# Performance work log

Measured on AMD Instinct MI355X. Metric: run time of the kernel, lower is better.

Reference implementation:

```python
import jax, jax.numpy as jnp
import numpy as np

HIDDEN = 1024
HEADS = 16
HEAD_DIM = HIDDEN // HEADS
SCALE = 1.0 / float(np.sqrt(HEAD_DIM))


def setup_inputs() -> dict:
    key = jax.random.key(0)
    k1, k2, k3, k4 = jax.random.split(key, 4)
    B, N, C = 4, 2048, HIDDEN
    x = jax.random.normal(k1, (B, N, C), dtype=jnp.float32)
    # nn.Linear(C, 3C, bias=False): y = x @ W_qkv where W_qkv is [C, 3C]
    w_qkv = jax.random.normal(k2, (C, 3 * C), dtype=jnp.float32) * (1.0 / np.sqrt(C))
    # nn.Linear(C, C) with bias
    w_out = jax.random.normal(k3, (C, C), dtype=jnp.float32) * (1.0 / np.sqrt(C))
    b_out = jax.random.normal(k4, (C,), dtype=jnp.float32) * 0.01
    return {"x": x, "w_qkv": w_qkv, "w_out": w_out, "b_out": b_out}


def reference(x, w_qkv, w_out, b_out):
    B, N, C = x.shape
    H, D = HEADS, HEAD_DIM
    qkv = jnp.einsum("bnc,cf->bnf", x, w_qkv)  # [B, N, 3C]
    qkv = qkv.reshape(B, N, 3, H, D).transpose(2, 0, 3, 1, 4)  # [3, B, H, N, D]
    q, k, v = qkv[0], qkv[1], qkv[2]
    attn = jnp.einsum("bhnd,bhmd->bhnm", q, k) * SCALE  # [B, H, N, N]
    attn = jax.nn.softmax(attn, axis=-1)
    # dropout is identity in eval mode
    out = jnp.einsum("bhnm,bhmd->bhnd", attn, v)  # [B, H, N, D]
    out = out.transpose(0, 2, 1, 3).reshape(B, N, C)
    return jnp.einsum("bnc,co->bno", out, w_out) + b_out
```

## Files before the change

### kernel.cpp

```cpp
#include <hip/hip_runtime.h>
#include <hip/hip_bf16.h>
#include <stdint.h>

#define SEQ   2048
#define NBH   64
#define DH    64
#define CH    1024
#define MTOT  8192
#define QSCALE 0.1803368801111204f

typedef __bf16 bf16_t;
typedef bf16_t bf16x8 __attribute__((ext_vector_type(8)));
typedef float  f32x4  __attribute__((ext_vector_type(4)));
typedef float  f32x16 __attribute__((ext_vector_type(16)));

__device__ __forceinline__ bf16_t to_bf16(float f) {
  uint32_t u = __builtin_bit_cast(uint32_t, f);
  uint16_t r = (uint16_t)((u + 0x7fffu + ((u >> 16) & 1u)) >> 16);
  return __builtin_bit_cast(bf16_t, r);
}

__device__ __forceinline__ void gload_lds16(const void* g, void* l) {
  __builtin_amdgcn_global_load_lds(
      (const __attribute__((address_space(1))) uint32_t*)g,
      (__attribute__((address_space(3))) uint32_t*)l, 16, 0, 0);
}

__device__ __forceinline__ f32x4 mfma_bf16(bf16x8 a, bf16x8 b, f32x4 c) {
  return __builtin_amdgcn_mfma_f32_16x16x32_bf16(a, b, c, 0, 0, 0);
}
__device__ __forceinline__ f32x16 mfma32_bf16(bf16x8 a, bf16x8 b, f32x16 c) {
  return __builtin_amdgcn_mfma_f32_32x32x16_bf16(a, b, c, 0, 0, 0);
}

__device__ __forceinline__ float exp2_fast(float x) {
#if __has_builtin(__builtin_amdgcn_exp2f)
  return __builtin_amdgcn_exp2f(x);
#else
  float r;
  asm("v_exp_f32 %0, %1\ns_nop 0" : "=v"(r) : "v"(x));
  return r;
#endif
}

__device__ __forceinline__ uint32_t cvt_pk_bf16(float lo, float hi) {
  uint32_t r;
  asm("v_cvt_pk_bf16_f32 %0, %1, %2" : "=v"(r) : "v"(lo), "v"(hi));
  return r;
}

__device__ __forceinline__ void permlane32_swap(uint32_t& a, uint32_t& b) {
  asm("s_nop 1\n\tv_permlane32_swap_b32 %0, %1\n\ts_nop 1" : "+v"(a), "+v"(b));
}

__global__ __launch_bounds__(256) void prep(
    const float* __restrict__ x, bf16_t* __restrict__ xb,
    const float* __restrict__ w_qkv, bf16_t* __restrict__ wqkvT,
    const float* __restrict__ w_out, bf16_t* __restrict__ woT) {
  __shared__ float t[64 * 65];
  const int tid = threadIdx.x;
  const int blk = blockIdx.x;
  if (blk < 2048) {
    int i = (blk * 256 + tid) * 8;
    const int stride = 2048 * 256 * 8;
    for (; i < MTOT * CH; i += stride) {
      const float4 f0 = *reinterpret_cast<const float4*>(x + i);
      const float4 f1 = *reinterpret_cast<const float4*>(x + i + 4);
      const uint4 pk = make_uint4(cvt_pk_bf16(f0.x, f0.y), cvt_pk_bf16(f0.z, f0.w),
                                  cvt_pk_bf16(f1.x, f1.y), cvt_pk_bf16(f1.z, f1.w));
      *reinterpret_cast<uint4*>(xb + i) = pk;
    }
    return;
  }
  const float* W; bf16_t* WT; int Nd, nx, bi;
  if (blk < 2048 + 768) { bi = blk - 2048; W = w_qkv; WT = wqkvT; Nd = 3 * CH; nx = 48; }
  else                  { bi = blk - 2816; W = w_out; WT = woT;   Nd = CH;     nx = 16; }
  const int n0 = (bi % nx) * 64, k0 = (bi / nx) * 64;
#pragma unroll
  for (int rr = 0; rr < 16; ++rr) {
    const int idx = rr * 256 + tid;
    const int r = idx >> 6, c = idx & 63;
    t[r * 65 + c] = W[(size_t)(k0 + r) * Nd + n0 + c];
  }
  __syncthreads();
#pragma unroll
  for (int rr = 0; rr < 16; ++rr) {
    const int idx = rr * 256 + tid;
    const int nr = idx >> 6, kc = idx & 63;
    WT[(size_t)(n0 + nr) * CH + k0 + kc] = to_bf16(t[kc * 65 + nr]);
  }
}


template <int EPI>
__global__ __launch_bounds__(256, 3) void gemm_bt(
    const bf16_t* __restrict__ A, const bf16_t* __restrict__ BT, int K, int nx,
    bf16_t* __restrict__ qb, bf16_t* __restrict__ kb, bf16_t* __restrict__ vb,
    const float* __restrict__ bias, float* __restrict__ out) {
  __shared__ __attribute__((aligned(16))) bf16_t lA[128 * 64];
  __shared__ __attribute__((aligned(16))) bf16_t lB[128 * 64];
  const int tid = threadIdx.x;
  const int lane = tid & 63;
  const int wv = tid >> 6;
  const int wm = wv >> 1, wn = wv & 1;

  const int nwg = gridDim.x;
  int bid = blockIdx.x;
  bid = (bid & 7) * (nwg >> 3) + (bid >> 3);
  const int m0 = (bid / nx) * 128, n0 = (bid % nx) * 128;

  const int l15 = lane & 15, l16 = lane >> 4;

  f32x4 acc[4][4] = {};

  const int srow = tid >> 3;
  const int sch = tid & 7;

  for (int kt = 0; kt < K; kt += 64) {
#pragma unroll
    for (int c = 0; c < 4; ++c) {
      const int row = c * 32 + srow;
      const int cs = sch ^ (row & 7);
      gload_lds16(A + (size_t)(m0 + row) * K + kt + cs * 8, &lA[c * 2048 + tid * 8]);
    }
#pragma unroll
    for (int c = 0; c < 4; ++c) {
      const int row = c * 32 + srow;
      const int cs = sch ^ (row & 7);
      gload_lds16(BT + (size_t)(n0 + row) * K + kt + cs * 8, &lB[c * 2048 + tid * 8]);
    }
    __syncthreads();
#pragma unroll
    for (int ks = 0; ks < 2; ++ks) {
      bf16x8 af[4], bfr[4];
#pragma unroll
      for (int i = 0; i < 4; ++i) {
        const int ar = wm * 64 + i * 16 + l15;
        const int cha = (ks * 4 + l16) ^ (ar & 7);
        af[i] = *reinterpret_cast<const bf16x8*>(&lA[ar * 64 + cha * 8]);
        const int br = wn * 64 + i * 16 + l15;
        const int chb = (ks * 4 + l16) ^ (br & 7);
        bfr[i] = *reinterpret_cast<const bf16x8*>(&lB[br * 64 + chb * 8]);
      }
#pragma unroll
      for (int i = 0; i < 4; ++i)
#pragma unroll
        for (int j = 0; j < 4; ++j)
          acc[i][j] = mfma_bf16(af[i], bfr[j], acc[i][j]);
    }
    __syncthreads();
  }

  if (EPI == 0) {
    const int f0 = n0 + wn * 64;
    const int three = f0 >> 10;
    if (three < 2) {
#pragma unroll
      for (int i = 0; i < 4; ++i) {
#pragma unroll
        for (int j = 0; j < 4; ++j) {
#pragma unroll
          for (int r = 0; r < 4; ++r) {
            const int m = m0 + wm * 64 + i * 16 + l16 * 4 + r;
            const int f = f0 + j * 16 + l15;
            const int h = (f >> 6) & 15, d = f & 63;
            const int bh = (m >> 11) * 16 + h;
            const int n = m & 2047;
            const float val = acc[i][j][r];
            if (three == 0)
              qb[((size_t)bh * SEQ + n) * DH + d] = to_bf16(val * QSCALE);
            else
              kb[((size_t)bh * SEQ + n) * DH + d] = to_bf16(val);
          }
        }
      }
    } else {
#pragma unroll
      for (int i = 0; i < 4; ++i) {
#pragma unroll
        for (int j = 0; j < 4; ++j) {
          const int m = m0 + wm * 64 + i * 16 + l16 * 4;
          const int f = f0 + j * 16 + l15;
          const int h = (f >> 6) & 15, d = f & 63;
          const int bh = (m >> 11) * 16 + h;
          const int n = m & 2047;
          const uint2 pk = make_uint2(cvt_pk_bf16(acc[i][j][0], acc[i][j][1]),
                                      cvt_pk_bf16(acc[i][j][2], acc[i][j][3]));
          *reinterpret_cast<uint2*>(&vb[((size_t)bh * DH + d) * SEQ + n]) = pk;
        }
      }
    }
  } else {
#pragma unroll
    for (int j = 0; j < 4; ++j) {
      const int cc = n0 + wn * 64 + j * 16 + l15;
      const float bb = bias[cc];
#pragma unroll
      for (int i = 0; i < 4; ++i) {
#pragma unroll
        for (int r = 0; r < 4; ++r) {
          const int m = m0 + wm * 64 + i * 16 + l16 * 4 + r;
          out[(size_t)m * CH + cc] = acc[i][j][r] + bb;
        }
      }
    }
  }
}

__global__ __launch_bounds__(256, 4) void attn_fwd(
    const bf16_t* __restrict__ Q, const bf16_t* __restrict__ K,
    const bf16_t* __restrict__ V, bf16_t* __restrict__ O) {
  __shared__ __attribute__((aligned(16))) bf16_t lK[2][64 * 64];
  __shared__ __attribute__((aligned(16))) bf16_t lV[2][64 * 64];
  const int tid = threadIdx.x;
  const int lane = tid & 63;
  const int wv = tid >> 6;
  const int l31 = lane & 31, hi = lane >> 5;

  const int lin = blockIdx.x;
  const int bh = (lin & 7) * 8 + ((lin >> 3) & 7);
  const int qb = lin >> 6;
  const int q0w = qb * 128 + wv * 32;

  const bf16_t* Qb = Q + (size_t)bh * SEQ * DH;
  const bf16_t* Kb = K + (size_t)bh * SEQ * DH;
  const bf16_t* Vb = V + (size_t)bh * DH * SEQ;

  bf16x8 qf[4];
#pragma unroll
  for (int ks = 0; ks < 4; ++ks)
    qf[ks] = *reinterpret_cast<const bf16x8*>(
        Qb + (size_t)(q0w + l31) * DH + ks * 16 + hi * 8);

  f32x16 o0 = {}, o1 = {};
  float rs0 = 0.f, rs1 = 0.f, rs2 = 0.f, rs3 = 0.f;

  const int srow = tid >> 3;
  const int sch = tid & 7;

  auto stage = [&](int buf, int kt0) {
#pragma unroll
    for (int c = 0; c < 2; ++c) {
      const int row = c * 32 + srow;
      const int cs = sch ^ (row & 7);
      gload_lds16(Kb + (size_t)(kt0 + row) * DH + cs * 8,
                  reinterpret_cast<char*>(&lK[buf][0]) + c * 4096 + tid * 16);
      gload_lds16(Vb + (size_t)row * SEQ + kt0 + cs * 8,
                  reinterpret_cast<char*>(&lV[buf][0]) + c * 4096 + tid * 16);
    }
  };

  stage(0, 0);
  __syncthreads();
  int cur = 0;

  for (int t = 0; t < SEQ / 64; ++t) {
    if (t + 1 < SEQ / 64) stage(cur ^ 1, (t + 1) * 64);

    f32x16 s0 = {}, s1 = {};
    __builtin_amdgcn_s_setprio(1);
#pragma unroll
    for (int ks = 0; ks < 4; ++ks) {
      {
        const int row = l31;
        const int ch = (ks * 2 + hi) ^ (row & 7);
        const bf16x8 kf = *reinterpret_cast<const bf16x8*>(
            reinterpret_cast<const char*>(&lK[cur][0]) + row * 128 + ch * 16);
        s0 = mfma32_bf16(kf, qf[ks], s0);
      }
      {
        const int row = 32 + l31;
        const int ch = (ks * 2 + hi) ^ (row & 7);
        const bf16x8 kf = *reinterpret_cast<const bf16x8*>(
            reinterpret_cast<const char*>(&lK[cur][0]) + row * 128 + ch * 16);
        s1 = mfma32_bf16(kf, qf[ks], s1);
      }
    }
    __builtin_amdgcn_s_setprio(0);

#pragma unroll
    for (int j = 0; j < 16; j += 4) {
      s0[j]     = exp2_fast(s0[j]);     rs0 += s0[j];
      s0[j + 1] = exp2_fast(s0[j + 1]); rs1 += s0[j + 1];
      s0[j + 2] = exp2_fast(s0[j + 2]); rs2 += s0[j + 2];
      s0[j + 3] = exp2_fast(s0[j + 3]); rs3 += s0[j + 3];
    }
#pragma unroll
    for (int j = 0; j < 16; j += 4) {
      s1[j]     = exp2_fast(s1[j]);     rs0 += s1[j];
      s1[j + 1] = exp2_fast(s1[j + 1]); rs1 += s1[j + 1];
      s1[j + 2] = exp2_fast(s1[j + 2]); rs2 += s1[j + 2];
      s1[j + 3] = exp2_fast(s1[j + 3]); rs3 += s1[j + 3];
    }

    bf16x8 pa[4];
    {
      uint32_t a0 = cvt_pk_bf16(s0[0], s0[1]),   b0 = cvt_pk_bf16(s0[4], s0[5]);
      uint32_t a1 = cvt_pk_bf16(s0[2], s0[3]),   b1 = cvt_pk_bf16(s0[6], s0[7]);
      uint32_t a2 = cvt_pk_bf16(s0[8], s0[9]),   b2 = cvt_pk_bf16(s0[12], s0[13]);
      uint32_t a3 = cvt_pk_bf16(s0[10], s0[11]), b3 = cvt_pk_bf16(s0[14], s0[15]);
      permlane32_swap(a0, b0);
      permlane32_swap(a1, b1);
      permlane32_swap(a2, b2);
      permlane32_swap(a3, b3);
      union { uint32_t u[4]; bf16x8 v; } ua, ub, uc, ud;
      ua.u[0] = a0; ua.u[1] = a1; ua.u[2] = b0; ua.u[3] = b1; pa[0] = ua.v;
      ub.u[0] = a2; ub.u[1] = a3; ub.u[2] = b2; ub.u[3] = b3; pa[1] = ub.v;
      uint32_t c0 = cvt_pk_bf16(s1[0], s1[1]),   d0 = cvt_pk_bf16(s1[4], s1[5]);
      uint32_t c1 = cvt_pk_bf16(s1[2], s1[3]),   d1 = cvt_pk_bf16(s1[6], s1[7]);
      uint32_t c2 = cvt_pk_bf16(s1[8], s1[9]),   d2 = cvt_pk_bf16(s1[12], s1[13]);
      uint32_t c3 = cvt_pk_bf16(s1[10], s1[11]), d3 = cvt_pk_bf16(s1[14], s1[15]);
      permlane32_swap(c0, d0);
      permlane32_swap(c1, d1);
      permlane32_swap(c2, d2);
      permlane32_swap(c3, d3);
      uc.u[0] = c0; uc.u[1] = c1; uc.u[2] = d0; uc.u[3] = d1; pa[2] = uc.v;
      ud.u[0] = c2; ud.u[1] = c3; ud.u[2] = d2; ud.u[3] = d3; pa[3] = ud.v;
    }

    __builtin_amdgcn_s_setprio(1);
#pragma unroll
    for (int tt = 0; tt < 4; ++tt) {
      {
        const int row = l31;
        const int ch = (tt * 2 + hi) ^ (row & 7);
        const bf16x8 vf = *reinterpret_cast<const bf16x8*>(
            reinterpret_cast<const char*>(&lV[cur][0]) + row * 128 + ch * 16);
        o0 = mfma32_bf16(pa[tt], vf, o0);
      }
      {
        const int row = 32 + l31;
        const int ch = (tt * 2 + hi) ^ (row & 7);
        const bf16x8 vf = *reinterpret_cast<const bf16x8*>(
            reinterpret_cast<const char*>(&lV[cur][0]) + row * 128 + ch * 16);
        o1 = mfma32_bf16(pa[tt], vf, o1);
      }
    }
    __builtin_amdgcn_s_setprio(0);

    __syncthreads();
    cur ^= 1;
  }

  const float rs = (rs0 + rs1) + (rs2 + rs3);
  uint32_t ra = __builtin_bit_cast(uint32_t, rs), rb2 = ra;
  permlane32_swap(ra, rb2);
  const float tot = __builtin_bit_cast(float, ra) + __builtin_bit_cast(float, rb2);
  const float rinv = 1.0f / tot;

  const int b = bh >> 4, h = bh & 15;
#pragma unroll
  for (int r = 0; r < 16; ++r) {
    const int qr = (r & 3) + 8 * (r >> 2) + 4 * hi;
    const float inv = __shfl(rinv, qr, 64);
    const size_t grow = (size_t)(b * SEQ + q0w + qr) * CH + h * DH;
    O[grow + l31]      = to_bf16(o0[r] * inv);
    O[grow + 32 + l31] = to_bf16(o1[r] * inv);
  }
}


extern "C" void kernel_launch(void* const* d_in, const int* in_sizes, int n_in,
                              void* d_out, int out_size, void* d_ws, size_t ws_size,
                              hipStream_t stream) {
  const float* x     = (const float*)d_in[0];
  const float* w_qkv = (const float*)d_in[1];
  const float* w_out = (const float*)d_in[2];
  const float* b_out = (const float*)d_in[3];
  float* out = (float*)d_out;

  char* ws = (char*)d_ws;
  bf16_t* xb    = (bf16_t*)(ws);
  bf16_t* wqkvT = (bf16_t*)(ws + 16777216);
  bf16_t* woT   = (bf16_t*)(ws + 23068672);
  bf16_t* Qb    = (bf16_t*)(ws + 25165824);
  bf16_t* Kb    = (bf16_t*)(ws + 41943040);
  bf16_t* Vb    = (bf16_t*)(ws + 58720256);
  bf16_t* Ab    = xb;

  prep<<<3072, 256, 0, stream>>>(x, xb, w_qkv, wqkvT, w_out, woT);

  gemm_bt<0><<<(3 * CH / 128) * (MTOT / 128), 256, 0, stream>>>(
      xb, wqkvT, CH, 3 * CH / 128, Qb, Kb, Vb, nullptr, nullptr);

  attn_fwd<<<1024, 256, 0, stream>>>(Qb, Kb, Vb, Ab);

  gemm_bt<1><<<(CH / 128) * (MTOT / 128), 256, 0, stream>>>(
      Ab, woT, CH, CH / 128, nullptr, nullptr, nullptr, b_out, out);
}
```

Before: 166.2 us.

## Software-pipeline PV matmul one tile behind QK and split K/V staging

Restructures the attention inner loop so the P·V MFMAs for tile t-1 are issued right after the QK^T MFMAs for tile t, letting the exp/convert work overlap with matrix ops. K and V staging are split: K is prefetched one tile ahead and V is loaded for the current tile, consumed one iteration later. The goal is to overlap softmax ALU work with MFMA and reduce stalls per iteration. This keeps pa live across iterations, which raises register pressure, and it relies on the barrier ordering of V buffer reuse.

```diff
diff --git a/kernel.cpp b/kernel.cpp
--- a/kernel.cpp
+++ b/kernel.cpp
@@ -158,7 +158,7 @@
 #pragma unroll
       for (int i = 0; i < 4; ++i) {
 #pragma unroll
-        for (int j = 0; j < 4; ++j) {
+      for (int j = 0; j < 4; ++j) {
 #pragma unroll
           for (int r = 0; r < 4; ++r) {
             const int m = m0 + wm * 64 + i * 16 + l16 * 4 + r;
@@ -234,28 +234,36 @@
 
   f32x16 o0 = {}, o1 = {};
   float rs0 = 0.f, rs1 = 0.f, rs2 = 0.f, rs3 = 0.f;
+  bf16x8 pa[4];
 
   const int srow = tid >> 3;
   const int sch = tid & 7;
 
-  auto stage = [&](int buf, int kt0) {
+  auto stageK = [&](int buf, int kt0) {
 #pragma unroll
     for (int c = 0; c < 2; ++c) {
       const int row = c * 32 + srow;
       const int cs = sch ^ (row & 7);
       gload_lds16(Kb + (size_t)(kt0 + row) * DH + cs * 8,
                   reinterpret_cast<char*>(&lK[buf][0]) + c * 4096 + tid * 16);
+    }
+  };
+  auto stageV = [&](int buf, int kt0) {
+#pragma unroll
+    for (int c = 0; c < 2; ++c) {
+      const int row = c * 32 + srow;
+      const int cs = sch ^ (row & 7);
       gload_lds16(Vb + (size_t)row * SEQ + kt0 + cs * 8,
                   reinterpret_cast<char*>(&lV[buf][0]) + c * 4096 + tid * 16);
     }
   };
 
-  stage(0, 0);
+  stageK(0, 0);
   __syncthreads();
-  int cur = 0;
 
   for (int t = 0; t < SEQ / 64; ++t) {
-    if (t + 1 < SEQ / 64) stage(cur ^ 1, (t + 1) * 64);
+    if (t + 1 < SEQ / 64) stageK((t + 1) & 1, (t + 1) * 64);
+    stageV(t & 1, t * 64);
 
     f32x16 s0 = {}, s1 = {};
     __builtin_amdgcn_s_setprio(1);
@@ -265,15 +273,33 @@
         const int row = l31;
         const int ch = (ks * 2 + hi) ^ (row & 7);
         const bf16x8 kf = *reinterpret_cast<const bf16x8*>(
-            reinterpret_cast<const char*>(&lK[cur][0]) + row * 128 + ch * 16);
+            reinterpret_cast<const char*>(&lK[t & 1][0]) + row * 128 + ch * 16);
         s0 = mfma32_bf16(kf, qf[ks], s0);
       }
       {
         const int row = 32 + l31;
         const int ch = (ks * 2 + hi) ^ (row & 7);
         const bf16x8 kf = *reinterpret_cast<const bf16x8*>(
-            reinterpret_cast<const char*>(&lK[cur][0]) + row * 128 + ch * 16);
+            reinterpret_cast<const char*>(&lK[t & 1][0]) + row * 128 + ch * 16);
         s1 = mfma32_bf16(kf, qf[ks], s1);
+      }
+    }
+    if (t) {
+      const char* vb0 = reinterpret_cast<const char*>(&lV[(t - 1) & 1][0]);
+#pragma unroll
+      for (int tt = 0; tt < 4; ++tt) {
+        {
+          const int row = l31;
+          const int ch = (tt * 2 + hi) ^ (row & 7);
+          const bf16x8 vf = *reinterpret_cast<const bf16x8*>(vb0 + row * 128 + ch * 16);
+          o0 = mfma32_bf16(pa[tt], vf, o0);
+        }
+        {
+          const int row = 32 + l31;
+          const int ch = (tt * 2 + hi) ^ (row & 7);
+          const bf16x8 vf = *reinterpret_cast<const bf16x8*>(vb0 + row * 128 + ch * 16);
+          o1 = mfma32_bf16(pa[tt], vf, o1);
+        }
       }
     }
     __builtin_amdgcn_s_setprio(0);
@@ -292,8 +318,6 @@
       s1[j + 2] = exp2_fast(s1[j + 2]); rs2 += s1[j + 2];
       s1[j + 3] = exp2_fast(s1[j + 3]); rs3 += s1[j + 3];
     }
-
-    bf16x8 pa[4];
     {
       uint32_t a0 = cvt_pk_bf16(s0[0], s0[1]),   b0 = cvt_pk_bf16(s0[4], s0[5]);
       uint32_t a1 = cvt_pk_bf16(s0[2], s0[3]),   b1 = cvt_pk_bf16(s0[6], s0[7]);
@@ -318,28 +342,28 @@
       ud.u[0] = c2; ud.u[1] = c3; ud.u[2] = d2; ud.u[3] = d3; pa[3] = ud.v;
     }
 
+    __syncthreads();
+  }
+
+  {
+    const char* vb0 = reinterpret_cast<const char*>(&lV[(SEQ / 64 - 1) & 1][0]);
     __builtin_amdgcn_s_setprio(1);
 #pragma unroll
     for (int tt = 0; tt < 4; ++tt) {
       {
         const int row = l31;
         const int ch = (tt * 2 + hi) ^ (row & 7);
-        const bf16x8 vf = *reinterpret_cast<const bf16x8*>(
-            reinterpret_cast<const char*>(&lV[cur][0]) + row * 128 + ch * 16);
+        const bf16x8 vf = *reinterpret_cast<const bf16x8*>(vb0 + row * 128 + ch * 16);
         o0 = mfma32_bf16(pa[tt], vf, o0);
       }
       {
         const int row = 32 + l31;
         const int ch = (tt * 2 + hi) ^ (row & 7);
-        const bf16x8 vf = *reinterpret_cast<const bf16x8*>(
-            reinterpret_cast<const char*>(&lV[cur][0]) + row * 128 + ch * 16);
+        const bf16x8 vf = *reinterpret_cast<const bf16x8*>(vb0 + row * 128 + ch * 16);
         o1 = mfma32_bf16(pa[tt], vf, o1);
       }
     }
     __builtin_amdgcn_s_setprio(0);
-
-    __syncthreads();
-    cur ^= 1;
   }
 
   const float rs = (rs0 + rs1) + (rs2 + rs3);
```

Result: no change. 169.4 us (+1.9%).

## Replace QKV GEMM with 256x256 8-wave double-buffered pipelined kernel

Applied to the files above, without the earlier changes.

The QKV projection GEMM now uses a dedicated kernel with 256x256 output tiles, 512 threads and a double-buffered LDS ring split into half-tiles. Loads for the next k-step are issued between the four compute phases, with explicit vmcnt waits, barriers and setprio around the MFMA bursts. The larger tiles are meant to raise arithmetic intensity and hide global-to-LDS latency. In exchange, 128 KB of LDS allows only one block per CU, and the 384-block grid may fill the 256 CUs unevenly. The output-projection GEMM is split into its own non-templated kernel with unchanged logic.

```diff
diff --git a/kernel.cpp b/kernel.cpp
--- a/kernel.cpp
+++ b/kernel.cpp
@@ -91,11 +91,152 @@
   }
 }
 
-
-template <int EPI>
-__global__ __launch_bounds__(256, 3) void gemm_bt(
+__global__ __launch_bounds__(512, 1) void gemm8p_qkv(
+    const bf16_t* __restrict__ A, const bf16_t* __restrict__ BT,
+    bf16_t* __restrict__ qb, bf16_t* __restrict__ kb, bf16_t* __restrict__ vb) {
+  __shared__ __attribute__((aligned(16))) bf16_t lA[2][2][128 * 64];
+  __shared__ __attribute__((aligned(16))) bf16_t lB[2][2][128 * 64];
+  const int tid = threadIdx.x;
+  const int lane = tid & 63;
+  const int wv = tid >> 6;
+  const int wr = wv >> 2, wc = wv & 3;
+  const int l15 = lane & 15, l16 = lane >> 4;
+
+  const int nwg = gridDim.x;
+  int bid = blockIdx.x;
+  bid = (bid & 7) * (nwg >> 3) + (bid >> 3);
+  const int m0 = (bid / 12) * 256, n0 = (bid % 12) * 256;
+
+  f32x4 acc[8][4] = {};
+
+  const int srow = tid >> 3;
+  const int sch = tid & 7;
+
+  auto stageA = [&](int pb, int mh, int kt) {
+#pragma unroll
+    for (int l = 0; l < 2; ++l) {
+      const int q = l * 64 + srow;
+      const int grow = m0 + ((q >> 6) << 7) + mh * 64 + (q & 63);
+      const int cs = sch ^ (q & 7);
+      gload_lds16(A + (size_t)grow * CH + kt + cs * 8,
+                  reinterpret_cast<char*>(&lA[pb][mh][0]) + l * 8192 + tid * 16);
+    }
+  };
+  auto stageB = [&](int pb, int nh, int kt) {
+#pragma unroll
+    for (int l = 0; l < 2; ++l) {
+      const int q = l * 64 + srow;
+      const int grow = n0 + ((q >> 5) << 6) + nh * 32 + (q & 31);
+      const int cs = sch ^ (q & 7);
+      gload_lds16(BT + (size_t)grow * CH + kt + cs * 8,
+                  reinterpret_cast<char*>(&lB[pb][nh][0]) + l * 8192 + tid * 16);
+    }
+  };
+
+#define VMB(N) asm volatile("s_waitcnt vmcnt(" #N ")\n\ts_barrier" ::: "memory")
+#define BARO() asm volatile("s_barrier" ::: "memory")
+
+#define PHASE(PB, MH, NH, STAGE_STMT)                                          \
+  {                                                                            \
+    const bf16_t* Ab_ = &lA[PB][MH][0];                                        \
+    const bf16_t* Bb_ = &lB[PB][NH][0];                                        \
+    bf16x8 af_[4][2], bf_[2][2];                                               \
+    _Pragma("unroll") for (int i = 0; i < 4; ++i) {                            \
+      const int q = wr * 64 + i * 16 + l15;                                    \
+      _Pragma("unroll") for (int kk = 0; kk < 2; ++kk) {                       \
+        const int ch = (kk * 4 + l16) ^ (q & 7);                               \
+        af_[i][kk] = *reinterpret_cast<const bf16x8*>(&Ab_[q * 64 + ch * 8]);  \
+      }                                                                        \
+    }                                                                          \
+    _Pragma("unroll") for (int j = 0; j < 2; ++j) {                            \
+      const int q = wc * 32 + j * 16 + l15;                                    \
+      _Pragma("unroll") for (int kk = 0; kk < 2; ++kk) {                       \
+        const int ch = (kk * 4 + l16) ^ (q & 7);                               \
+        bf_[j][kk] = *reinterpret_cast<const bf16x8*>(&Bb_[q * 64 + ch * 8]);  \
+      }                                                                        \
+    }                                                                          \
+    STAGE_STMT;                                                                \
+    __builtin_amdgcn_s_setprio(1);                                             \
+    _Pragma("unroll") for (int i = 0; i < 4; ++i)                              \
+      _Pragma("unroll") for (int j = 0; j < 2; ++j) {                          \
+        acc[MH * 4 + i][NH * 2 + j] =                                          \
+            mfma_bf16(af_[i][0], bf_[j][0], acc[MH * 4 + i][NH * 2 + j]);      \
+        acc[MH * 4 + i][NH * 2 + j] =                                          \
+            mfma_bf16(af_[i][1], bf_[j][1], acc[MH * 4 + i][NH * 2 + j]);      \
+      }                                                                        \
+    __builtin_amdgcn_s_setprio(0);                                             \
+  }
+
+  stageA(0, 0, 0);
+  stageB(0, 0, 0);
+  stageA(0, 1, 0);
+  stageB(0, 1, 0);
+
+  for (int kt = 0; kt < 15; ++kt) {
+    const int pb = kt & 1, pn = pb ^ 1;
+    const int kn = (kt + 1) * 64;
+    if (pb == 0) {
+      VMB(4); PHASE(0, 0, 0, stageA(1, 0, kn));
+      VMB(4); PHASE(0, 1, 0, stageB(1, 0, kn));
+      VMB(4); PHASE(0, 0, 1, stageA(1, 1, kn));
+      BARO(); PHASE(0, 1, 1, stageB(1, 1, kn));
+    } else {
+      VMB(4); PHASE(1, 0, 0, stageA(0, 0, kn));
+      VMB(4); PHASE(1, 1, 0, stageB(0, 0, kn));
+      VMB(4); PHASE(1, 0, 1, stageA(0, 1, kn));
+      BARO(); PHASE(1, 1, 1, stageB(0, 1, kn));
+    }
+  }
+  VMB(4); PHASE(1, 0, 0, );
+  VMB(2); PHASE(1, 1, 0, );
+  VMB(0); PHASE(1, 0, 1, );
+  BARO(); PHASE(1, 1, 1, );
+
+#undef PHASE
+#undef VMB
+#undef BARO
+
+  const int three = n0 >> 10;
+  if (three < 2) {
+#pragma unroll
+    for (int mf = 0; mf < 8; ++mf) {
+#pragma unroll
+      for (int nf = 0; nf < 4; ++nf) {
+#pragma unroll
+        for (int r = 0; r < 4; ++r) {
+          const int m = m0 + wr * 128 + (mf >> 2) * 64 + (mf & 3) * 16 + l16 * 4 + r;
+          const int f = n0 + wc * 64 + (nf >> 1) * 32 + (nf & 1) * 16 + l15;
+          const int h = (f >> 6) & 15, d = f & 63;
+          const int bh = (m >> 11) * 16 + h;
+          const int n = m & 2047;
+          const float val = acc[mf][nf][r];
+          if (three == 0)
+            qb[((size_t)bh * SEQ + n) * DH + d] = to_bf16(val * QSCALE);
+          else
+            kb[((size_t)bh * SEQ + n) * DH + d] = to_bf16(val);
+        }
+      }
+    }
+  } else {
+#pragma unroll
+    for (int mf = 0; mf < 8; ++mf) {
+#pragma unroll
+      for (int nf = 0; nf < 4; ++nf) {
+        const int m = m0 + wr * 128 + (mf >> 2) * 64 + (mf & 3) * 16 + l16 * 4;
+        const int f = n0 + wc * 64 + (nf >> 1) * 32 + (nf & 1) * 16 + l15;
+        const int h = (f >> 6) & 15, d = f & 63;
+        const int bh = (m >> 11) * 16 + h;
+        const int n = m & 2047;
+        const uint2 pk = make_uint2(cvt_pk_bf16(acc[mf][nf][0], acc[mf][nf][1]),
+                                    cvt_pk_bf16(acc[mf][nf][2], acc[mf][nf][3]));
+        *reinterpret_cast<uint2*>(&vb[((size_t)bh * DH + d) * SEQ + n]) = pk;
+      }
+    }
+  }
+}
+
+__global__ __launch_bounds__(256, 3) void gemm_out(
     const bf16_t* __restrict__ A, const bf16_t* __restrict__ BT, int K, int nx,
-    bf16_t* __restrict__ qb, bf16_t* __restrict__ kb, bf16_t* __restrict__ vb,
     const float* __restrict__ bias, float* __restrict__ out) {
   __shared__ __attribute__((aligned(16))) bf16_t lA[128 * 64];
   __shared__ __attribute__((aligned(16))) bf16_t lB[128 * 64];
@@ -151,57 +292,16 @@
     __syncthreads();
   }
 
-  if (EPI == 0) {
-    const int f0 = n0 + wn * 64;
-    const int three = f0 >> 10;
-    if (three < 2) {
-#pragma unroll
-      for (int i = 0; i < 4; ++i) {
-#pragma unroll
-        for (int j = 0; j < 4; ++j) {
-#pragma unroll
-          for (int r = 0; r < 4; ++r) {
-            const int m = m0 + wm * 64 + i * 16 + l16 * 4 + r;
-            const int f = f0 + j * 16 + l15;
-            const int h = (f >> 6) & 15, d = f & 63;
-            const int bh = (m >> 11) * 16 + h;
-            const int n = m & 2047;
-            const float val = acc[i][j][r];
-            if (three == 0)
-              qb[((size_t)bh * SEQ + n) * DH + d] = to_bf16(val * QSCALE);
-            else
-              kb[((size_t)bh * SEQ + n) * DH + d] = to_bf16(val);
-          }
-        }
-      }
-    } else {
-#pragma unroll
-      for (int i = 0; i < 4; ++i) {
-#pragma unroll
-        for (int j = 0; j < 4; ++j) {
-          const int m = m0 + wm * 64 + i * 16 + l16 * 4;
-          const int f = f0 + j * 16 + l15;
-          const int h = (f >> 6) & 15, d = f & 63;
-          const int bh = (m >> 11) * 16 + h;
-          const int n = m & 2047;
-          const uint2 pk = make_uint2(cvt_pk_bf16(acc[i][j][0], acc[i][j][1]),
-                                      cvt_pk_bf16(acc[i][j][2], acc[i][j][3]));
-          *reinterpret_cast<uint2*>(&vb[((size_t)bh * DH + d) * SEQ + n]) = pk;
-        }
-      }
-    }
-  } else {
-#pragma unroll
-    for (int j = 0; j < 4; ++j) {
-      const int cc = n0 + wn * 64 + j * 16 + l15;
-      const float bb = bias[cc];
-#pragma unroll
-      for (int i = 0; i < 4; ++i) {
-#pragma unroll
-        for (int r = 0; r < 4; ++r) {
-          const int m = m0 + wm * 64 + i * 16 + l16 * 4 + r;
-          out[(size_t)m * CH + cc] = acc[i][j][r] + bb;
-        }
+#pragma unroll
+  for (int j = 0; j < 4; ++j) {
+    const int cc = n0 + wn * 64 + j * 16 + l15;
+    const float bb = bias[cc];
+#pragma unroll
+    for (int i = 0; i < 4; ++i) {
+#pragma unroll
+      for (int r = 0; r < 4; ++r) {
+        const int m = m0 + wm * 64 + i * 16 + l16 * 4 + r;
+        out[(size_t)m * CH + cc] = acc[i][j][r] + bb;
       }
     }
   }
@@ -380,11 +480,11 @@
 
   prep<<<3072, 256, 0, stream>>>(x, xb, w_qkv, wqkvT, w_out, woT);
 
-  gemm_bt<0><<<(3 * CH / 128) * (MTOT / 128), 256, 0, stream>>>(
-      xb, wqkvT, CH, 3 * CH / 128, Qb, Kb, Vb, nullptr, nullptr);
+  gemm8p_qkv<<<(MTOT / 256) * (3 * CH / 256), 512, 0, stream>>>(
+      xb, wqkvT, Qb, Kb, Vb);
 
   attn_fwd<<<1024, 256, 0, stream>>>(Qb, Kb, Vb, Ab);
 
-  gemm_bt<1><<<(CH / 128) * (MTOT / 128), 256, 0, stream>>>(
-      Ab, woT, CH, CH / 128, nullptr, nullptr, nullptr, b_out, out);
-}
+  gemm_out<<<(CH / 128) * (MTOT / 128), 256, 0, stream>>>(
+      Ab, woT, CH, CH / 128, b_out, out);
+}
```

After: 458.0 us. 176% more time.
